# Performance work log

Measured on AMD Instinct MI355X. Metric: run time of the kernel, lower is better.

## Reference

```python
import jax, jax.numpy as jnp
import numpy as np
from jax import lax

INPUT, HIDDEN, OUTPUT = 128, 1024, 128
BATCH, T_STEPS = 256, 512


def _uniform(key, shape, fan_in):
    bound = 1.0 / np.sqrt(fan_in)
    return jax.random.uniform(key, shape, jnp.float32, -bound, bound)


def setup_inputs() -> dict:
    key = jax.random.key(0)
    ks = jax.random.split(key, 7)
    return {
        "x_0": jax.random.normal(ks[0], (BATCH, INPUT), jnp.float32),
        "W_i2h": _uniform(ks[1], (INPUT, HIDDEN), INPUT),
        "b_i2h": _uniform(ks[2], (HIDDEN,), INPUT),
        "W_h2h": _uniform(ks[3], (HIDDEN, HIDDEN), HIDDEN),
        "b_h2h": _uniform(ks[4], (HIDDEN,), HIDDEN),
        "W_h2o": _uniform(ks[5], (HIDDEN, OUTPUT), HIDDEN),
        "b_h2o": _uniform(ks[6], (OUTPUT,), HIDDEN),
        "T": T_STEPS,
    }


def reference(x_0, W_i2h, b_i2h, W_h2h, b_h2h, W_h2o, b_h2o, T):
    batch = x_0.shape[0]
    h0 = jnp.zeros((batch, W_h2h.shape[0]), x_0.dtype)

    def step(carry, _):
        x, h = carry
        # hidden_pre = i2h(x) + h2h(h); hidden = tanh(hidden_pre)
        h = jnp.tanh(x @ W_i2h + b_i2h + h @ W_h2h + b_h2h)
        x_out = h @ W_h2o + b_h2o  # fed back as next input
        return (x_out, h), x_out

    _, ys = lax.scan(step, (x_0, h0), None, length=T - 1)
    # trajectory[0] = x_0, trajectory[t+1] = x_output at step t
    return jnp.concatenate([x_0[None], ys], axis=0)  # [T, B, output]
```

## Files before the change

### kernel.cpp

```cpp
#include <hip/hip_runtime.h>
#include <cstdint>
#include <cstddef>


#define BATCH  256
#define INPUT  128
#define HIDDEN 1024
#define OUTPUT 128
#define TSTEPS 512
#define NCAT   1152
#define NTILE  72
#define GROUPS 16
#define MEMB   16
#define NSLOT  4

#define WS_WFRAG 0u
#define WS_BEFF  2621440u
#define WS_HBUF  2629632u
#define WS_BAR   4726784u
#define BAR_U32S 768

typedef _Float16 f16;
typedef _Float16 v8h __attribute__((ext_vector_type(8)));
typedef float    v4f __attribute__((ext_vector_type(4)));

__device__ __forceinline__ float fast_tanh(float x){
  float e = __expf(2.0f * x);
  return (e - 1.0f) / (e + 1.0f);
}

__global__ void k_bias(const float* __restrict__ bi2h, const float* __restrict__ bh2h,
                       const float* __restrict__ bh2o, const float* __restrict__ Wi2h,
                       float* __restrict__ beff){
  int n = blockIdx.x*256 + threadIdx.x;
  if (n >= 1168) return;
  float v = 0.f;
  if (n < HIDDEN){
    v = bi2h[n] + bh2h[n];
    for (int j=0;j<INPUT;j++) v += bh2o[j]*Wi2h[j*HIDDEN + n];
  } else if (n < NCAT){
    v = bh2o[n - HIDDEN];
  }
  beff[n] = v;
}

__global__ void k_h1(const float* __restrict__ x0, const float* __restrict__ Wi2h,
                     const float* __restrict__ bi2h, const float* __restrict__ bh2h,
                     f16* __restrict__ hbuf){
  int idx = blockIdx.x*256 + threadIdx.x;
  int m = idx >> 10, n = idx & 1023;
  float acc = bi2h[n] + bh2h[n];
  const float* xr = x0 + m*INPUT;
  for (int j=0;j<INPUT;j++) acc += xr[j]*Wi2h[j*HIDDEN + n];
  hbuf[idx] = (f16)fast_tanh(acc);
}

__global__ void k_copy0(const float* __restrict__ x0, float* __restrict__ out){
  int i = blockIdx.x*256 + threadIdx.x;
  out[i] = x0[i];
}

__global__ void k_wfrag(const float* __restrict__ Wh2h, const float* __restrict__ Wh2o,
                        const float* __restrict__ Wi2h, f16* __restrict__ Wfrag){
  int gid = blockIdx.x*256 + threadIdx.x;
  int lane = gid & 63;
  int fi = gid >> 6;
  int c = fi % 5, kk = (fi/5) & 7, wv = (fi/40) & 3, mem = fi/160;
  int k0 = wv*256 + kk*32 + (lane>>4)*8;
  int n  = mem*NTILE + c*16 + (lane & 15);
  f16 vals[8];
  if (n >= NCAT){
    #pragma unroll
    for (int j=0;j<8;j++) vals[j] = (f16)0.f;
  } else if (n >= HIDDEN){
    #pragma unroll
    for (int j=0;j<8;j++) vals[j] = (f16)Wh2o[(k0+j)*OUTPUT + (n-HIDDEN)];
  } else {
    float acc[8];
    #pragma unroll
    for (int j=0;j<8;j++) acc[j] = Wh2h[(k0+j)*HIDDEN + n];
    for (int q=0;q<INPUT;q++){
      float wi = Wi2h[q*HIDDEN + n];
      #pragma unroll
      for (int j=0;j<8;j++) acc[j] += Wh2o[(k0+j)*OUTPUT + q]*wi;
    }
    #pragma unroll
    for (int j=0;j<8;j++) vals[j] = (f16)acc[j];
  }
  v8h pack;
  #pragma unroll
  for (int j=0;j<8;j++) pack[j] = vals[j];
  *(v8h*)(Wfrag + (size_t)gid*8) = pack;
}

__global__ void __launch_bounds__(256, 1)
k_rnn(const f16* __restrict__ Wfrag, const float* __restrict__ beff,
      f16* __restrict__ hbuf, unsigned int* __restrict__ bar,
      float* __restrict__ out){
  extern __shared__ char lds_raw[];
  float*    red    = (float*)lds_raw;
  unsigned* s_slot = (unsigned*)(lds_raw + 16384);

  const int tid  = threadIdx.x;
  const int lane = tid & 63;
  const int wv   = tid >> 6;

  if (tid == 0){
    unsigned xcc;
    asm volatile("s_getreg_b32 %0, hwreg(HW_REG_XCC_ID)" : "=s"(xcc));
    xcc &= 7;
    unsigned slot = atomicAdd(&bar[512 + xcc*32], 1u);
    *s_slot = xcc*32 + (slot & 31u);
  }
  __syncthreads();
  const unsigned sid = *s_slot;
  const int g   = sid >> 4;
  const int mem = sid & 15;
  if (g >= GROUPS) return;
  const int m0   = g * 16;
  const int n0   = mem * NTILE;
  const int quad = lane >> 4;
  const int l15  = lane & 15;

  v8h bw[8][5];
  {
    const f16* wp = Wfrag + ((size_t)((mem*4 + wv)*40)*64 + lane)*8;
    #pragma unroll
    for (int kk=0;kk<8;kk++)
      #pragma unroll
      for (int c=0;c<5;c++)
        bw[kk][c] = *(const v8h*)(wp + (size_t)((kk*5+c)*64)*8);
  }

  const int kbase = wv*256;
  unsigned int* cnt = bar + g*32;

  for (int t=1; t<TSTEPS; ++t){
    const f16* hin  = hbuf + (size_t)((t-1)&(NSLOT-1))*(BATCH*HIDDEN);
    f16*       hout = hbuf + (size_t)(t&(NSLOT-1))*(BATCH*HIDDEN);

    v8h af[8];
    {
      const v8h* abase = (const v8h*)(hin + (size_t)(m0 + l15)*HIDDEN + kbase + quad*8);
      #pragma unroll
      for (int kk=0;kk<8;kk++)
        af[kk] = abase[kk*4];
    }

    v4f acc[5];
    #pragma unroll
    for (int c=0;c<5;c++){ v4f z = {0.f,0.f,0.f,0.f}; acc[c] = z; }

    #pragma unroll
    for (int kk=0;kk<8;kk++){
      #pragma unroll
      for (int c=0;c<5;c++)
        acc[c] = __builtin_amdgcn_mfma_f32_16x16x32_f16(af[kk], bw[kk][c], acc[c], 0,0,0);
    }

    #pragma unroll
    for (int c=0;c<5;c++){
      int owner = c & 3;
      if (wv != owner){
        int rank = (wv > owner) ? wv-1 : wv;
        *(v4f*)(red + ((size_t)(c*3 + rank)*64 + lane)*4) = acc[c];
      }
    }
    __syncthreads();

    #pragma unroll
    for (int c=0;c<5;c++){
      if ((c & 3) == wv){
        int colT = c*16 + l15;
        int col  = n0 + colT;
        if (col < HIDDEN && colT < NTILE){
          v4f s = acc[c];
          #pragma unroll
          for (int r=0;r<3;r++) s += *(const v4f*)(red + ((size_t)(c*3 + r)*64 + lane)*4);
          float b = beff[col];
          #pragma unroll
          for (int r=0;r<4;r++){
            float v = fast_tanh(s[r] + b);
            hout[(size_t)(m0 + quad*4 + r)*HIDDEN + col] = (f16)v;
          }
        }
      }
    }
    __syncthreads();
    if (tid == 0){
      atomicAdd(cnt, 1u);
    }
    #pragma unroll
    for (int c=0;c<5;c++){
      if ((c & 3) == wv){
        int colT = c*16 + l15;
        int col  = n0 + colT;
        if (col >= HIDDEN && colT < NTILE){
          v4f s = acc[c];
          #pragma unroll
          for (int r=0;r<3;r++) s += *(const v4f*)(red + ((size_t)(c*3 + r)*64 + lane)*4);
          float b = beff[col];
          float* op = out + (size_t)t*(BATCH*OUTPUT) + (col - HIDDEN);
          #pragma unroll
          for (int r=0;r<4;r++)
            op[(size_t)(m0 + quad*4 + r)*OUTPUT] = s[r] + b;
        }
      }
    }
    if (tid == 0){
      unsigned tries = 0;
      while (__hip_atomic_load(cnt, __ATOMIC_RELAXED, __HIP_MEMORY_SCOPE_AGENT)
             < (unsigned)(MEMB*t) && tries < 2048u){
        __builtin_amdgcn_s_sleep(1);
        ++tries;
      }
    }
    __syncthreads();
  }
}

extern "C" void kernel_launch(void* const* d_in, const int* in_sizes, int n_in,
                              void* d_out, int out_size, void* d_ws, size_t ws_size,
                              hipStream_t stream){
  const float* x0   = (const float*)d_in[0];
  const float* Wi2h = (const float*)d_in[1];
  const float* bi2h = (const float*)d_in[2];
  const float* Wh2h = (const float*)d_in[3];
  const float* bh2h = (const float*)d_in[4];
  const float* Wh2o = (const float*)d_in[5];
  const float* bh2o = (const float*)d_in[6];
  float* out = (float*)d_out;
  char* ws = (char*)d_ws;

  f16*          Wfrag = (f16*)(ws + WS_WFRAG);
  float*        beff  = (float*)(ws + WS_BEFF);
  f16*          hbuf  = (f16*)(ws + WS_HBUF);
  unsigned int* bar   = (unsigned int*)(ws + WS_BAR);

  hipMemsetAsync(bar, 0, BAR_U32S*sizeof(unsigned int), stream);
  k_bias <<<5,    256, 0, stream>>>(bi2h, bh2h, bh2o, Wi2h, beff);
  k_h1   <<<1024, 256, 0, stream>>>(x0, Wi2h, bi2h, bh2h, hbuf);
  k_copy0<<<128,  256, 0, stream>>>(x0, out);
  k_wfrag<<<640,  256, 0, stream>>>(Wh2h, Wh2o, Wi2h, Wfrag);

  hipFuncSetAttribute((const void*)k_rnn, hipFuncAttributeMaxDynamicSharedMemorySize, 98304);
  k_rnn<<<256, 256, 98304, stream>>>(Wfrag, beff, hbuf, bar, out);
}
```

Baseline: 1.724 ms.

## Replace counter barrier with per-member flags polled by every wave

Swaps the shared atomic-add counter barrier for per-block flag slots, each written with an atomic store of the step index. Every wave now polls all 16 flags with a ballot and no sleep, so the trailing __syncthreads is gone. The epilogue is also simplified by precomputing column indices, biases and output offsets outside the time loop. The aim is to cut barrier latency and atomic contention per step, at the cost of more polling traffic and a bounded spin that could break out early without the per-step block sync.

Result: slower. 1.955 ms (+13.4%).

```diff
diff --git a/kernel.cpp b/kernel.cpp
--- a/kernel.cpp
+++ b/kernel.cpp
@@ -133,7 +133,19 @@
   }
 
   const int kbase = wv*256;
-  unsigned int* cnt = bar + g*32;
+  unsigned int* flags = bar + g*32;
+
+  const int  colA   = n0 + wv*16 + l15;
+  const bool A_hid  = (colA < HIDDEN);
+  const float biasA = beff[colA];
+  const bool has4   = (wv == 0) && (l15 < 8);
+  const int  col4   = n0 + 64 + l15;
+  const bool hid4   = (col4 < HIDDEN);
+  const float bias4 = has4 ? beff[col4] : 0.f;
+  const size_t hoffA = (size_t)(m0 + quad*4)*HIDDEN + colA;
+  const size_t yoffA = (size_t)(m0 + quad*4)*OUTPUT + (colA - HIDDEN);
+  const size_t hoff4 = (size_t)(m0 + quad*4)*HIDDEN + col4;
+  const size_t yoff4 = (size_t)(m0 + quad*4)*OUTPUT + (col4 - HIDDEN);
 
   for (int t=1; t<TSTEPS; ++t){
     const f16* hin  = hbuf + (size_t)((t-1)&(NSLOT-1))*(BATCH*HIDDEN);
@@ -168,54 +180,52 @@
     }
     __syncthreads();
 
-    #pragma unroll
-    for (int c=0;c<5;c++){
-      if ((c & 3) == wv){
-        int colT = c*16 + l15;
-        int col  = n0 + colT;
-        if (col < HIDDEN && colT < NTILE){
-          v4f s = acc[c];
-          #pragma unroll
-          for (int r=0;r<3;r++) s += *(const v4f*)(red + ((size_t)(c*3 + r)*64 + lane)*4);
-          float b = beff[col];
-          #pragma unroll
-          for (int r=0;r<4;r++){
-            float v = fast_tanh(s[r] + b);
-            hout[(size_t)(m0 + quad*4 + r)*HIDDEN + col] = (f16)v;
-          }
-        }
-      }
+    v4f sA = acc[wv];
+    #pragma unroll
+    for (int r=0;r<3;r++) sA += *(const v4f*)(red + ((size_t)(wv*3 + r)*64 + lane)*4);
+    v4f s4 = acc[4];
+    if (wv == 0){
+      #pragma unroll
+      for (int r=0;r<3;r++) s4 += *(const v4f*)(red + ((size_t)(4*3 + r)*64 + lane)*4);
+    }
+
+    if (A_hid){
+      #pragma unroll
+      for (int r=0;r<4;r++)
+        hout[hoffA + (size_t)r*HIDDEN] = (f16)fast_tanh(sA[r] + biasA);
+    }
+    if (has4 && hid4){
+      #pragma unroll
+      for (int r=0;r<4;r++)
+        hout[hoff4 + (size_t)r*HIDDEN] = (f16)fast_tanh(s4[r] + bias4);
     }
     __syncthreads();
     if (tid == 0){
-      atomicAdd(cnt, 1u);
-    }
-    #pragma unroll
-    for (int c=0;c<5;c++){
-      if ((c & 3) == wv){
-        int colT = c*16 + l15;
-        int col  = n0 + colT;
-        if (col >= HIDDEN && colT < NTILE){
-          v4f s = acc[c];
-          #pragma unroll
-          for (int r=0;r<3;r++) s += *(const v4f*)(red + ((size_t)(c*3 + r)*64 + lane)*4);
-          float b = beff[col];
-          float* op = out + (size_t)t*(BATCH*OUTPUT) + (col - HIDDEN);
-          #pragma unroll
-          for (int r=0;r<4;r++)
-            op[(size_t)(m0 + quad*4 + r)*OUTPUT] = s[r] + b;
-        }
+      __hip_atomic_store(&flags[mem], (unsigned)t, __ATOMIC_RELAXED, __HIP_MEMORY_SCOPE_AGENT);
+    }
+
+    if (!A_hid){
+      float* op = out + (size_t)t*(BATCH*OUTPUT) + yoffA;
+      #pragma unroll
+      for (int r=0;r<4;r++) op[(size_t)r*OUTPUT] = sA[r] + biasA;
+    }
+    if (has4 && !hid4){
+      float* op = out + (size_t)t*(BATCH*OUTPUT) + yoff4;
+      #pragma unroll
+      for (int r=0;r<4;r++) op[(size_t)r*OUTPUT] = s4[r] + bias4;
+    }
+
+    {
+      unsigned tries = 0;
+      for (;;){
+        unsigned f = 0;
+        if (lane < MEMB)
+          f = __hip_atomic_load(&flags[lane], __ATOMIC_RELAXED, __HIP_MEMORY_SCOPE_AGENT);
+        unsigned long long b = __ballot((lane >= MEMB) || (f >= (unsigned)t));
+        if (b == ~0ull || ++tries >= 4096u) break;
       }
-    }
-    if (tid == 0){
-      unsigned tries = 0;
-      while (__hip_atomic_load(cnt, __ATOMIC_RELAXED, __HIP_MEMORY_SCOPE_AGENT)
-             < (unsigned)(MEMB*t) && tries < 2048u){
-        __builtin_amdgcn_s_sleep(1);
-        ++tries;
-      }
-    }
-    __syncthreads();
+      asm volatile("" ::: "memory");
+    }
   }
 }
 
```
